# Optimization experiments

Hardware: AMD Instinct MI355X
Metric: run time of the kernel (lower is better)

Reference implementation:

```python
import math
import jax, jax.numpy as jnp
import numpy as np

N_HEAD = 16
N_HEAD_KV = 4
HEAD_DIM = 64
WINDOW = 512  # (window, 0) sliding-window causal, as in flash_attn window_size
ROPE_BASE = 10000.0


def _rope(x):
    """Rotate-half RoPE. x: (B, T, H, D)."""
    T, D = x.shape[1], x.shape[3]
    half = D // 2
    inv_freq = 1.0 / (ROPE_BASE ** (jnp.arange(half, dtype=jnp.float32) / half))
    ang = jnp.arange(T, dtype=jnp.float32)[:, None] * inv_freq[None, :]  # (T, half)
    cos = jnp.concatenate([jnp.cos(ang), jnp.cos(ang)], axis=-1)[None, :, None, :]
    sin = jnp.concatenate([jnp.sin(ang), jnp.sin(ang)], axis=-1)[None, :, None, :]
    x1, x2 = jnp.split(x, 2, axis=-1)
    rot = jnp.concatenate([-x2, x1], axis=-1)
    return x * cos.astype(x.dtype) + rot * sin.astype(x.dtype)


def setup_inputs() -> dict:
    key = jax.random.key(0)
    ks = jax.random.split(key, 7)
    B, T, C = 2, 2048, 1024
    Ckv = N_HEAD_KV * HEAD_DIM
    x = jax.random.normal(ks[0], (B, T, C), dtype=jnp.float32)
    seq_lengths = jax.random.randint(ks[1], (B,), T // 2, T + 1, dtype=jnp.int32)
    s = 0.02
    Wq = jax.random.normal(ks[2], (C, C), dtype=jnp.float32) * s
    Wk = jax.random.normal(ks[3], (C, Ckv), dtype=jnp.float32) * s
    Wv = jax.random.normal(ks[4], (C, Ckv), dtype=jnp.float32) * s
    Wo = jax.random.normal(ks[5], (C, C), dtype=jnp.float32) * s
    return {"x": x, "seq_lengths": seq_lengths, "Wq": Wq, "Wk": Wk, "Wv": Wv, "Wo": Wo}


def reference(x, seq_lengths, Wq, Wk, Wv, Wo):
    B, T, C = x.shape
    scale = 1.0 / math.sqrt(HEAD_DIM)
    q = (x @ Wq).reshape(B, T, N_HEAD, HEAD_DIM)
    k = (x @ Wk).reshape(B, T, N_HEAD_KV, HEAD_DIM)
    v = (x @ Wv).reshape(B, T, N_HEAD_KV, HEAD_DIM)
    q = _rope(q)
    k = _rope(k)
    # GQA: repeat_interleave KV heads up to N_HEAD
    rep = N_HEAD // N_HEAD_KV
    k = jnp.repeat(k, rep, axis=2)
    v = jnp.repeat(v, rep, axis=2)
    scores = jnp.einsum("bqhd,bkhd->bhqk", q, k) * scale  # (B,H,T,T)
    pos = jnp.arange(T)
    causal = pos[None, :] <= pos[:, None]                      # k <= q
    window = pos[None, :] >= (pos[:, None] - WINDOW)           # k >= q - W
    key_valid = pos[None, :] < seq_lengths[:, None]            # (B,T)
    mask = (causal & window)[None, None, :, :] & key_valid[:, None, None, :]
    scores = jnp.where(mask, scores, jnp.float32(-1e9))
    attn = jax.nn.softmax(scores, axis=-1)
    out = jnp.einsum("bhqk,bkhd->bqhd", attn, v)
    # padded query positions are zeroed (pad_input semantics in the varlen path)
    q_valid = (pos[None, :] < seq_lengths[:, None]).astype(out.dtype)
    out = out * q_valid[:, :, None, None]
    return out.reshape(B, T, C) @ Wo
```

## Files before the change

kernel.cpp:

```cpp
#include <hip/hip_runtime.h>


using bf16x8 = __attribute__((ext_vector_type(8))) short;
using f32x4  = __attribute__((ext_vector_type(4))) float;

#define B_   2
#define T_   2048
#define H_   16
#define HKV_ 4
#define D_   64
#define WIN_ 512

#define QSCALE_ 0.18033688011112042f
#define LOG2_1E4_OVER32_ 0.41524101186092029f

__device__ __forceinline__ unsigned short f2b(float f) {
  union { float f; unsigned u; } v; v.f = f;
  unsigned r = v.u + 0x7FFFu + ((v.u >> 16) & 1u);
  return (unsigned short)(r >> 16);
}
__device__ __forceinline__ unsigned short f2b_fast(float f) {
  union { float f; unsigned u; } v; v.f = f;
  return (unsigned short)((v.u + 0x8000u) >> 16);
}

typedef const __attribute__((address_space(1))) void* gas_ptr;
typedef __attribute__((address_space(3))) void* las_ptr;
__device__ __forceinline__ void gl_lds16(const void* g, void* l) {
  __builtin_amdgcn_global_load_lds((gas_ptr)g, (las_ptr)l, 16, 0, 0);
}

__global__ __launch_bounds__(256) void prep_kernel(
    const float* __restrict__ x,
    const float* __restrict__ Wq, const float* __restrict__ Wk,
    const float* __restrict__ Wv, const float* __restrict__ Wo,
    unsigned short* __restrict__ xb,
    unsigned short* __restrict__ wqT, unsigned short* __restrict__ wkT,
    unsigned short* __restrict__ wvT, unsigned short* __restrict__ woT) {
  int bx = blockIdx.x;
  if (bx < 4096) {
    int i = bx * 256 + threadIdx.x;
    float4 v = ((const float4*)x)[i];
    ushort4 o; o.x = f2b(v.x); o.y = f2b(v.y); o.z = f2b(v.z); o.w = f2b(v.w);
    ((ushort4*)xb)[i] = o;
    return;
  }
  int id = bx - 4096;
  const float* W; unsigned short* WT; int N, n0, k0;
  if (id < 1024)      { W = Wq; WT = wqT; N = 1024; }
  else if (id < 2048) { W = Wo; WT = woT; N = 1024; id -= 1024; }
  else if (id < 2304) { W = Wk; WT = wkT; N = 256;  id -= 2048; }
  else                { W = Wv; WT = wvT; N = 256;  id -= 2304; }
  if (N == 1024) { n0 = (id & 31) * 32; k0 = (id >> 5) * 32; }
  else           { n0 = (id & 7)  * 32; k0 = (id >> 3) * 32; }
  __shared__ float tile[32][33];
  int tx = threadIdx.x & 31, ty = threadIdx.x >> 5;
#pragma unroll
  for (int yy = 0; yy < 32; yy += 8)
    tile[ty + yy][tx] = W[(size_t)(k0 + ty + yy) * N + n0 + tx];
  __syncthreads();
#pragma unroll
  for (int yy = 0; yy < 32; yy += 8)
    WT[(size_t)(n0 + ty + yy) * 1024 + k0 + tx] = f2b(tile[tx][ty + yy]);
}

__global__ __launch_bounds__(256) void gemm_qkv(
    const unsigned short* __restrict__ A,
    const unsigned short* __restrict__ WqT,
    const unsigned short* __restrict__ WkT,
    const unsigned short* __restrict__ WvT,
    unsigned short* __restrict__ qb,
    unsigned short* __restrict__ kbuf,
    unsigned short* __restrict__ vbT) {
  const int K = 1024;
  __shared__ unsigned short lA[2][64 * 64];
  __shared__ unsigned short lB[2][128 * 64];
  int tid = threadIdx.x, l = tid & 63, w = tid >> 6;
  int wr = w >> 1, wc = w & 1;
  int m0 = blockIdx.x * 64;
  int n0 = blockIdx.y * 128;
  const unsigned short* Bt; int nloc;
  if (n0 < 1024)      { Bt = WqT; nloc = n0; }
  else if (n0 < 1280) { Bt = WkT; nloc = n0 - 1024; }
  else                { Bt = WvT; nloc = n0 - 1280; }

  f32x4 acc[2][4] = {};

  int scol = (((l & 7) ^ (l >> 3)) << 3);
  const unsigned short* ga = A  + (size_t)(m0   + w * 16 + (l >> 3)) * K + scol;
  const unsigned short* gb = Bt + (size_t)(nloc + w * 32 + (l >> 3)) * K + scol;

#define STG(BUF, KOFF)                                                         \
  {                                                                            \
    gl_lds16(ga + (KOFF),                  &lA[BUF][(w * 16) * 64]);           \
    gl_lds16(ga + 8 * K + (KOFF),          &lA[BUF][(w * 16 + 8) * 64]);       \
    _Pragma("unroll")                                                          \
    for (int j = 0; j < 4; ++j)                                                \
      gl_lds16(gb + j * 8 * K + (KOFF),    &lB[BUF][(w * 32 + j * 8) * 64]);   \
  }

  STG(0, 0)
  for (int it = 0; it < 16; ++it) {
    int buf = it & 1;
    if (it < 15) {
      STG(buf ^ 1, (it + 1) * 64)
      asm volatile("s_waitcnt vmcnt(6)" ::: "memory");
    } else {
      asm volatile("s_waitcnt vmcnt(0)" ::: "memory");
    }
    __builtin_amdgcn_sched_barrier(0);
    __builtin_amdgcn_s_barrier();

    bf16x8 af[2][2], bfr[4][2];
#pragma unroll
    for (int mf = 0; mf < 2; ++mf) {
      int row = wr * 32 + mf * 16 + (l & 15);
#pragma unroll
      for (int ks = 0; ks < 2; ++ks)
        af[mf][ks] = *(const bf16x8*)(
            &lA[buf][row * 64 + (((ks * 4 + (l >> 4)) ^ (row & 7)) << 3)]);
    }
#pragma unroll
    for (int nf = 0; nf < 4; ++nf) {
      int row = wc * 64 + nf * 16 + (l & 15);
#pragma unroll
      for (int ks = 0; ks < 2; ++ks)
        bfr[nf][ks] = *(const bf16x8*)(
            &lB[buf][row * 64 + (((ks * 4 + (l >> 4)) ^ (row & 7)) << 3)]);
    }
    __builtin_amdgcn_s_setprio(1);
#pragma unroll
    for (int mf = 0; mf < 2; ++mf)
#pragma unroll
      for (int nf = 0; nf < 4; ++nf) {
        acc[mf][nf] = __builtin_amdgcn_mfma_f32_16x16x32_bf16(af[mf][0], bfr[nf][0], acc[mf][nf], 0, 0, 0);
        acc[mf][nf] = __builtin_amdgcn_mfma_f32_16x16x32_bf16(af[mf][1], bfr[nf][1], acc[mf][nf], 0, 0, 0);
      }
    __builtin_amdgcn_s_setprio(0);
    __builtin_amdgcn_s_barrier();
  }
#undef STG

  int colbase = n0 + wc * 64;
  int rowbase = m0 + wr * 32;

  if (n0 < 1280) {
    float qs = (n0 < 1024) ? QSCALE_ : 1.0f;
#pragma unroll
    for (int nf = 0; nf < 2; ++nf) {
      int dd = nf * 16 + (l & 15);
      float inv = exp2f(-(float)dd * LOG2_1E4_OVER32_);
#pragma unroll
      for (int mf = 0; mf < 2; ++mf) {
#pragma unroll
        for (int i = 0; i < 4; ++i) {
          int t = (rowbase + mf * 16 + ((l >> 4) << 2) + i) & 2047;
          float sn, cs;
          __sincosf((float)t * inv, &sn, &cs);
          float x1 = acc[mf][nf][i], x2 = acc[mf][nf + 2][i];
          acc[mf][nf][i]     = (x1 * cs - x2 * sn) * qs;
          acc[mf][nf + 2][i] = (x2 * cs + x1 * sn) * qs;
        }
      }
    }
  }

#pragma unroll
  for (int mf = 0; mf < 2; ++mf)
#pragma unroll
    for (int nf = 0; nf < 4; ++nf) {
      int n    = colbase + nf * 16 + (l & 15);
      int mrow = rowbase + mf * 16 + ((l >> 4) << 2);
      int b = mrow >> 11, t = mrow & 2047;
      if (n < 1024) {
        int h = n >> 6, d = n & 63;
        size_t base = ((size_t)(b * 16 + h) * 2048 + t) * 64 + d;
#pragma unroll
        for (int i = 0; i < 4; ++i) qb[base + (size_t)i * 64] = f2b(acc[mf][nf][i]);
      } else if (n < 1280) {
        int hh = (n - 1024) >> 6, d = n & 63;
        size_t base = ((size_t)(b * 4 + hh) * 2048 + t) * 64 + d;
#pragma unroll
        for (int i = 0; i < 4; ++i) kbuf[base + (size_t)i * 64] = f2b(acc[mf][nf][i]);
      } else {
        int hh = (n - 1280) >> 6, d = n & 63;
        size_t base = ((size_t)((b * 4 + hh) * 64 + d)) * 2048 + t;
        ushort4 pk;
        pk.x = f2b(acc[mf][nf][0]); pk.y = f2b(acc[mf][nf][1]);
        pk.z = f2b(acc[mf][nf][2]); pk.w = f2b(acc[mf][nf][3]);
        *(ushort4*)(&vbT[base]) = pk;
      }
    }
}

__global__ __launch_bounds__(512, 4) void attn_kernel(
    const unsigned short* __restrict__ qb,
    const unsigned short* __restrict__ kb,
    const unsigned short* __restrict__ vbT,
    const int* __restrict__ seqlen,
    unsigned short* __restrict__ att) {
  __shared__ unsigned short kl[2][64 * 64];
  __shared__ unsigned short vt[2][64 * 64];
  __shared__ unsigned short pl[8][16 * 68];

  int bx = blockIdx.x;
  int g  = bx & 7;
  int wi = bx >> 3;
  int b  = g >> 2;
  int hk = g & 3;
  int h  = hk * 4 + (wi & 3);
  int qt = wi >> 2;
  int tid = threadIdx.x, l = tid & 63, w = tid >> 6;
  int q0 = qt << 7;
  int r0 = q0 + w * 16;
  int slen = seqlen[b];

  const unsigned short* qbase = qb  + ((size_t)(b * 16 + h)  * 2048) * 64;
  const unsigned short* kbase = kb  + ((size_t)(b * 4  + hk) * 2048) * 64;
  const unsigned short* vbase = vbT + ((size_t)(b * 4  + hk) * 64)   * 2048;

  bf16x8 aq[2];
#pragma unroll
  for (int s = 0; s < 2; ++s)
    aq[s] = *(const bf16x8*)(qbase + (size_t)(r0 + (l & 15)) * 64 + s * 32 + (l >> 4) * 8);

  f32x4 o[4] = {};
  float lp[4] = {0.f, 0.f, 0.f, 0.f};

  int lo = q0 >= WIN_ ? q0 - WIN_ : 0;
  int nt = (q0 + 128 - lo) >> 6;

  int srow = (w << 3) + (l >> 3);
  int scol = (((l & 7) ^ (l >> 3)) << 3);
  const unsigned short* ksrc = kbase + (size_t)srow * 64   + scol;
  const unsigned short* vsrc = vbase + (size_t)srow * 2048 + scol;

#define STAGE(BUF, KB0)                                                        \
  {                                                                            \
    gl_lds16(ksrc + (size_t)(KB0) * 64, &kl[BUF][w * 512]);                    \
    gl_lds16(vsrc + (KB0),              &vt[BUF][w * 512]);                    \
  }

  STAGE(0, lo)
  __syncthreads();

  for (int it = 0; it < nt; ++it) {
    int kb0 = lo + (it << 6);
    int cur = it & 1;
    if (it + 1 < nt) STAGE(cur ^ 1, kb0 + 64)

    if (kb0 <= r0 + 15 && kb0 + 63 >= r0 - WIN_) {
      f32x4 sa[4];
      __builtin_amdgcn_s_setprio(1);
#pragma unroll
      for (int nf = 0; nf < 4; ++nf) {
        int row = nf * 16 + (l & 15);
        const unsigned short* kp0 =
            &kl[cur][row * 64 + (((l >> 4)       ^ (l & 7)) << 3)];
        const unsigned short* kp1 =
            &kl[cur][row * 64 + (((4 + (l >> 4)) ^ (l & 7)) << 3)];
        f32x4 z = {};
        z = __builtin_amdgcn_mfma_f32_16x16x32_bf16(aq[0], *(const bf16x8*)kp0, z, 0, 0, 0);
        z = __builtin_amdgcn_mfma_f32_16x16x32_bf16(aq[1], *(const bf16x8*)kp1, z, 0, 0, 0);
        sa[nf] = z;
      }
      __builtin_amdgcn_s_setprio(0);

      bool noMask = (kb0 + 63 <= r0) && (kb0 >= r0 - 497);
      if (!noMask) {
#pragma unroll
        for (int nf = 0; nf < 4; ++nf) {
          int key = kb0 + nf * 16 + (l & 15);
#pragma unroll
          for (int i = 0; i < 4; ++i) {
            int qr = r0 + (l >> 4) * 4 + i;
            sa[nf][i] = (key <= qr && key >= qr - WIN_) ? sa[nf][i] : -1e30f;
          }
        }
      }

#pragma unroll
      for (int nf = 0; nf < 4; ++nf)
#pragma unroll
        for (int i = 0; i < 4; ++i) {
          float p = exp2f(sa[nf][i]);
          lp[i] += p;
          pl[w][((l >> 4) * 4 + i) * 68 + nf * 16 + (l & 15)] = f2b_fast(p);
        }

      bf16x8 ap0 = *(const bf16x8*)(&pl[w][(l & 15) * 68 + (l >> 4) * 8]);
      bf16x8 ap1 = *(const bf16x8*)(&pl[w][(l & 15) * 68 + 32 + (l >> 4) * 8]);

      __builtin_amdgcn_s_setprio(1);
#pragma unroll
      for (int df = 0; df < 4; ++df) {
        int row = df * 16 + (l & 15);
        const unsigned short* vp0 =
            &vt[cur][row * 64 + (((l >> 4)       ^ (l & 7)) << 3)];
        const unsigned short* vp1 =
            &vt[cur][row * 64 + (((4 + (l >> 4)) ^ (l & 7)) << 3)];
        o[df] = __builtin_amdgcn_mfma_f32_16x16x32_bf16(ap0, *(const bf16x8*)vp0, o[df], 0, 0, 0);
        o[df] = __builtin_amdgcn_mfma_f32_16x16x32_bf16(ap1, *(const bf16x8*)vp1, o[df], 0, 0, 0);
      }
      __builtin_amdgcn_s_setprio(0);
    }
    __syncthreads();
  }
#undef STAGE

#pragma unroll
  for (int off = 1; off <= 8; off <<= 1)
#pragma unroll
    for (int i = 0; i < 4; ++i)
      lp[i] += __shfl_xor(lp[i], off);

#pragma unroll
  for (int i = 0; i < 4; ++i) {
    int r = r0 + (l >> 4) * 4 + i;
    float inv = (r < slen && lp[i] > 0.f) ? 1.0f / lp[i] : 0.f;
#pragma unroll
    for (int df = 0; df < 4; ++df)
      att[((size_t)(b * 2048 + r)) * 1024 + h * 64 + df * 16 + (l & 15)] =
          f2b(o[df][i] * inv);
  }
}

__global__ __launch_bounds__(256) void gemm_out(
    const unsigned short* __restrict__ A,
    const unsigned short* __restrict__ Bt,
    float* __restrict__ C) {
  const int K = 1024;
  __shared__ unsigned short lA[2][64 * 64];
  __shared__ unsigned short lB[2][128 * 64];
  int tid = threadIdx.x, l = tid & 63, w = tid >> 6;
  int wr = w >> 1, wc = w & 1;
  int m0 = blockIdx.x * 64;
  int n0 = blockIdx.y * 128;

  f32x4 acc[2][4] = {};

  int scol = (((l & 7) ^ (l >> 3)) << 3);
  const unsigned short* ga = A  + (size_t)(m0 + w * 16 + (l >> 3)) * K + scol;
  const unsigned short* gb = Bt + (size_t)(n0 + w * 32 + (l >> 3)) * K + scol;

#define STG(BUF, KOFF)                                                         \
  {                                                                            \
    gl_lds16(ga + (KOFF),                  &lA[BUF][(w * 16) * 64]);           \
    gl_lds16(ga + 8 * K + (KOFF),          &lA[BUF][(w * 16 + 8) * 64]);       \
    _Pragma("unroll")                                                          \
    for (int j = 0; j < 4; ++j)                                                \
      gl_lds16(gb + j * 8 * K + (KOFF),    &lB[BUF][(w * 32 + j * 8) * 64]);   \
  }

  STG(0, 0)
  for (int it = 0; it < 16; ++it) {
    int buf = it & 1;
    if (it < 15) {
      STG(buf ^ 1, (it + 1) * 64)
      asm volatile("s_waitcnt vmcnt(6)" ::: "memory");
    } else {
      asm volatile("s_waitcnt vmcnt(0)" ::: "memory");
    }
    __builtin_amdgcn_sched_barrier(0);
    __builtin_amdgcn_s_barrier();

    bf16x8 af[2][2], bfr[4][2];
#pragma unroll
    for (int mf = 0; mf < 2; ++mf) {
      int row = wr * 32 + mf * 16 + (l & 15);
#pragma unroll
      for (int ks = 0; ks < 2; ++ks)
        af[mf][ks] = *(const bf16x8*)(
            &lA[buf][row * 64 + (((ks * 4 + (l >> 4)) ^ (row & 7)) << 3)]);
    }
#pragma unroll
    for (int nf = 0; nf < 4; ++nf) {
      int row = wc * 64 + nf * 16 + (l & 15);
#pragma unroll
      for (int ks = 0; ks < 2; ++ks)
        bfr[nf][ks] = *(const bf16x8*)(
            &lB[buf][row * 64 + (((ks * 4 + (l >> 4)) ^ (row & 7)) << 3)]);
    }
    __builtin_amdgcn_s_setprio(1);
#pragma unroll
    for (int mf = 0; mf < 2; ++mf)
#pragma unroll
      for (int nf = 0; nf < 4; ++nf) {
        acc[mf][nf] = __builtin_amdgcn_mfma_f32_16x16x32_bf16(af[mf][0], bfr[nf][0], acc[mf][nf], 0, 0, 0);
        acc[mf][nf] = __builtin_amdgcn_mfma_f32_16x16x32_bf16(af[mf][1], bfr[nf][1], acc[mf][nf], 0, 0, 0);
      }
    __builtin_amdgcn_s_setprio(0);
    __builtin_amdgcn_s_barrier();
  }
#undef STG

  int colbase = n0 + wc * 64;
  int rowbase = m0 + wr * 32;
#pragma unroll
  for (int mf = 0; mf < 2; ++mf)
#pragma unroll
    for (int nf = 0; nf < 4; ++nf) {
      int n    = colbase + nf * 16 + (l & 15);
      int mrow = rowbase + mf * 16 + ((l >> 4) << 2);
#pragma unroll
      for (int i = 0; i < 4; ++i)
        C[(size_t)(mrow + i) * 1024 + n] = acc[mf][nf][i];
    }
}

extern "C" void kernel_launch(void* const* d_in, const int* in_sizes, int n_in,
                              void* d_out, int out_size, void* d_ws, size_t ws_size,
                              hipStream_t stream) {
  const float* x  = (const float*)d_in[0];
  const int*   sl = (const int*)d_in[1];
  const float* Wq = (const float*)d_in[2];
  const float* Wk = (const float*)d_in[3];
  const float* Wv = (const float*)d_in[4];
  const float* Wo = (const float*)d_in[5];
  float* out = (float*)d_out;

  char* p = (char*)d_ws;
  unsigned short* xb  = (unsigned short*)p; p += (size_t)4096 * 1024 * 2;
  unsigned short* wqT = (unsigned short*)p; p += (size_t)1024 * 1024 * 2;
  unsigned short* wkT = (unsigned short*)p; p += (size_t)256  * 1024 * 2;
  unsigned short* wvT = (unsigned short*)p; p += (size_t)256  * 1024 * 2;
  unsigned short* woT = (unsigned short*)p; p += (size_t)1024 * 1024 * 2;
  unsigned short* qb  = (unsigned short*)p; p += (size_t)B_ * H_   * T_ * D_ * 2;
  unsigned short* kbf = (unsigned short*)p; p += (size_t)B_ * HKV_ * T_ * D_ * 2;
  unsigned short* vbT = (unsigned short*)p; p += (size_t)B_ * HKV_ * D_ * T_ * 2;
  unsigned short* att = (unsigned short*)p; p += (size_t)4096 * 1024 * 2;

  prep_kernel<<<6656, 256, 0, stream>>>(x, Wq, Wk, Wv, Wo, xb, wqT, wkT, wvT, woT);
  gemm_qkv<<<dim3(64, 12), 256, 0, stream>>>(xb, wqT, wkT, wvT, qb, kbf, vbT);
  attn_kernel<<<512, 512, 0, stream>>>(qb, kbf, vbT, sl, att);
  gemm_out<<<dim3(64, 8), 256, 0, stream>>>(att, woT, out);
}
```

Measured before the change: 69.47 us.

## Skip padded rows in projection GEMMs and attention using sequence lengths

Each GEMM block whose 64-row tile starts at or beyond its batch's sequence length skips the K loop and its RoPE epilogue, storing zero accumulators instead. The attention kernel zero-fills its output and returns early for query tiles entirely past the sequence length, and caps the key-tile loop at the last valid row. The attention loop also swaps __syncthreads for explicit vmcnt waits plus s_barrier, so the next K/V tile's load stays in flight while the current one is used. The aim is to avoid computing rows that the reference masks or zeroes. The cost is extra branching and a dependence on seqlen inside every kernel.

```diff
diff --git a/kernel.cpp b/kernel.cpp
--- a/kernel.cpp
+++ b/kernel.cpp
@@ -69,6 +69,7 @@
     const unsigned short* __restrict__ WqT,
     const unsigned short* __restrict__ WkT,
     const unsigned short* __restrict__ WvT,
+    const int* __restrict__ seqlen,
     unsigned short* __restrict__ qb,
     unsigned short* __restrict__ kbuf,
     unsigned short* __restrict__ vbT) {
@@ -85,6 +86,7 @@
   else                { Bt = WvT; nloc = n0 - 1280; }
 
   f32x4 acc[2][4] = {};
+  bool dead = (m0 & 2047) >= seqlen[m0 >> 11];
 
   int scol = (((l & 7) ^ (l >> 3)) << 3);
   const unsigned short* ga = A  + (size_t)(m0   + w * 16 + (l >> 3)) * K + scol;
@@ -99,52 +101,54 @@
       gl_lds16(gb + j * 8 * K + (KOFF),    &lB[BUF][(w * 32 + j * 8) * 64]);   \
   }
 
-  STG(0, 0)
-  for (int it = 0; it < 16; ++it) {
-    int buf = it & 1;
-    if (it < 15) {
-      STG(buf ^ 1, (it + 1) * 64)
-      asm volatile("s_waitcnt vmcnt(6)" ::: "memory");
-    } else {
-      asm volatile("s_waitcnt vmcnt(0)" ::: "memory");
-    }
-    __builtin_amdgcn_sched_barrier(0);
-    __builtin_amdgcn_s_barrier();
-
-    bf16x8 af[2][2], bfr[4][2];
-#pragma unroll
-    for (int mf = 0; mf < 2; ++mf) {
-      int row = wr * 32 + mf * 16 + (l & 15);
-#pragma unroll
-      for (int ks = 0; ks < 2; ++ks)
-        af[mf][ks] = *(const bf16x8*)(
-            &lA[buf][row * 64 + (((ks * 4 + (l >> 4)) ^ (row & 7)) << 3)]);
-    }
-#pragma unroll
-    for (int nf = 0; nf < 4; ++nf) {
-      int row = wc * 64 + nf * 16 + (l & 15);
-#pragma unroll
-      for (int ks = 0; ks < 2; ++ks)
-        bfr[nf][ks] = *(const bf16x8*)(
-            &lB[buf][row * 64 + (((ks * 4 + (l >> 4)) ^ (row & 7)) << 3)]);
-    }
-    __builtin_amdgcn_s_setprio(1);
-#pragma unroll
-    for (int mf = 0; mf < 2; ++mf)
+  if (!dead) {
+    STG(0, 0)
+    for (int it = 0; it < 16; ++it) {
+      int buf = it & 1;
+      if (it < 15) {
+        STG(buf ^ 1, (it + 1) * 64)
+        asm volatile("s_waitcnt vmcnt(6)" ::: "memory");
+      } else {
+        asm volatile("s_waitcnt vmcnt(0)" ::: "memory");
+      }
+      __builtin_amdgcn_sched_barrier(0);
+      __builtin_amdgcn_s_barrier();
+
+      bf16x8 af[2][2], bfr[4][2];
+#pragma unroll
+      for (int mf = 0; mf < 2; ++mf) {
+        int row = wr * 32 + mf * 16 + (l & 15);
+#pragma unroll
+        for (int ks = 0; ks < 2; ++ks)
+          af[mf][ks] = *(const bf16x8*)(
+              &lA[buf][row * 64 + (((ks * 4 + (l >> 4)) ^ (row & 7)) << 3)]);
+      }
 #pragma unroll
       for (int nf = 0; nf < 4; ++nf) {
-        acc[mf][nf] = __builtin_amdgcn_mfma_f32_16x16x32_bf16(af[mf][0], bfr[nf][0], acc[mf][nf], 0, 0, 0);
-        acc[mf][nf] = __builtin_amdgcn_mfma_f32_16x16x32_bf16(af[mf][1], bfr[nf][1], acc[mf][nf], 0, 0, 0);
-      }
-    __builtin_amdgcn_s_setprio(0);
-    __builtin_amdgcn_s_barrier();
+        int row = wc * 64 + nf * 16 + (l & 15);
+#pragma unroll
+        for (int ks = 0; ks < 2; ++ks)
+          bfr[nf][ks] = *(const bf16x8*)(
+              &lB[buf][row * 64 + (((ks * 4 + (l >> 4)) ^ (row & 7)) << 3)]);
+      }
+      __builtin_amdgcn_s_setprio(1);
+#pragma unroll
+      for (int mf = 0; mf < 2; ++mf)
+#pragma unroll
+        for (int nf = 0; nf < 4; ++nf) {
+          acc[mf][nf] = __builtin_amdgcn_mfma_f32_16x16x32_bf16(af[mf][0], bfr[nf][0], acc[mf][nf], 0, 0, 0);
+          acc[mf][nf] = __builtin_amdgcn_mfma_f32_16x16x32_bf16(af[mf][1], bfr[nf][1], acc[mf][nf], 0, 0, 0);
+        }
+      __builtin_amdgcn_s_setprio(0);
+      __builtin_amdgcn_s_barrier();
+    }
   }
 #undef STG
 
   int colbase = n0 + wc * 64;
   int rowbase = m0 + wr * 32;
 
-  if (n0 < 1280) {
+  if (n0 < 1280 && !dead) {
     float qs = (n0 < 1024) ? QSCALE_ : 1.0f;
 #pragma unroll
     for (int nf = 0; nf < 2; ++nf) {
@@ -215,6 +219,16 @@
   int r0 = q0 + w * 16;
   int slen = seqlen[b];
 
+  if (q0 >= slen) {
+    int r = q0 + (tid >> 2);
+    int c = (tid & 3) * 16;
+    size_t base = ((size_t)(b * 2048 + r)) * 1024 + h * 64 + c;
+    ushort4 z = {0, 0, 0, 0};
+#pragma unroll
+    for (int j = 0; j < 4; ++j) *(ushort4*)(&att[base + j * 4]) = z;
+    return;
+  }
+
   const unsigned short* qbase = qb  + ((size_t)(b * 16 + h)  * 2048) * 64;
   const unsigned short* kbase = kb  + ((size_t)(b * 4  + hk) * 2048) * 64;
   const unsigned short* vbase = vbT + ((size_t)(b * 4  + hk) * 64)   * 2048;
@@ -228,7 +242,8 @@
   float lp[4] = {0.f, 0.f, 0.f, 0.f};
 
   int lo = q0 >= WIN_ ? q0 - WIN_ : 0;
-  int nt = (q0 + 128 - lo) >> 6;
+  int hi_row = min(q0 + 127, slen - 1);
+  int nt = ((hi_row - lo) >> 6) + 1;
 
   int srow = (w << 3) + (l >> 3);
   int scol = (((l & 7) ^ (l >> 3)) << 3);
@@ -242,12 +257,18 @@
   }
 
   STAGE(0, lo)
-  __syncthreads();
 
   for (int it = 0; it < nt; ++it) {
     int kb0 = lo + (it << 6);
     int cur = it & 1;
-    if (it + 1 < nt) STAGE(cur ^ 1, kb0 + 64)
+    if (it + 1 < nt) {
+      STAGE(cur ^ 1, kb0 + 64)
+      asm volatile("s_waitcnt vmcnt(2)" ::: "memory");
+    } else {
+      asm volatile("s_waitcnt vmcnt(0)" ::: "memory");
+    }
+    __builtin_amdgcn_sched_barrier(0);
+    __builtin_amdgcn_s_barrier();
 
     if (kb0 <= r0 + 15 && kb0 + 63 >= r0 - WIN_) {
       f32x4 sa[4];
@@ -304,7 +325,7 @@
       }
       __builtin_amdgcn_s_setprio(0);
     }
-    __syncthreads();
+    __builtin_amdgcn_s_barrier();
   }
 #undef STAGE
 
@@ -328,6 +349,7 @@
 __global__ __launch_bounds__(256) void gemm_out(
     const unsigned short* __restrict__ A,
     const unsigned short* __restrict__ Bt,
+    const int* __restrict__ seqlen,
     float* __restrict__ C) {
   const int K = 1024;
   __shared__ unsigned short lA[2][64 * 64];
@@ -338,6 +360,7 @@
   int n0 = blockIdx.y * 128;
 
   f32x4 acc[2][4] = {};
+  bool dead = (m0 & 2047) >= seqlen[m0 >> 11];
 
   int scol = (((l & 7) ^ (l >> 3)) << 3);
   const unsigned short* ga = A  + (size_t)(m0 + w * 16 + (l >> 3)) * K + scol;
@@ -352,45 +375,47 @@
       gl_lds16(gb + j * 8 * K + (KOFF),    &lB[BUF][(w * 32 + j * 8) * 64]);   \
   }
 
-  STG(0, 0)
-  for (int it = 0; it < 16; ++it) {
-    int buf = it & 1;
-    if (it < 15) {
-      STG(buf ^ 1, (it + 1) * 64)
-      asm volatile("s_waitcnt vmcnt(6)" ::: "memory");
-    } else {
-      asm volatile("s_waitcnt vmcnt(0)" ::: "memory");
-    }
-    __builtin_amdgcn_sched_barrier(0);
-    __builtin_amdgcn_s_barrier();
-
-    bf16x8 af[2][2], bfr[4][2];
-#pragma unroll
-    for (int mf = 0; mf < 2; ++mf) {
-      int row = wr * 32 + mf * 16 + (l & 15);
-#pragma unroll
-      for (int ks = 0; ks < 2; ++ks)
-        af[mf][ks] = *(const bf16x8*)(
-            &lA[buf][row * 64 + (((ks * 4 + (l >> 4)) ^ (row & 7)) << 3)]);
-    }
-#pragma unroll
-    for (int nf = 0; nf < 4; ++nf) {
-      int row = wc * 64 + nf * 16 + (l & 15);
-#pragma unroll
-      for (int ks = 0; ks < 2; ++ks)
-        bfr[nf][ks] = *(const bf16x8*)(
-            &lB[buf][row * 64 + (((ks * 4 + (l >> 4)) ^ (row & 7)) << 3)]);
-    }
-    __builtin_amdgcn_s_setprio(1);
-#pragma unroll
-    for (int mf = 0; mf < 2; ++mf)
+  if (!dead) {
+    STG(0, 0)
+    for (int it = 0; it < 16; ++it) {
+      int buf = it & 1;
+      if (it < 15) {
+        STG(buf ^ 1, (it + 1) * 64)
+        asm volatile("s_waitcnt vmcnt(6)" ::: "memory");
+      } else {
+        asm volatile("s_waitcnt vmcnt(0)" ::: "memory");
+      }
+      __builtin_amdgcn_sched_barrier(0);
+      __builtin_amdgcn_s_barrier();
+
+      bf16x8 af[2][2], bfr[4][2];
+#pragma unroll
+      for (int mf = 0; mf < 2; ++mf) {
+        int row = wr * 32 + mf * 16 + (l & 15);
+#pragma unroll
+        for (int ks = 0; ks < 2; ++ks)
+          af[mf][ks] = *(const bf16x8*)(
+              &lA[buf][row * 64 + (((ks * 4 + (l >> 4)) ^ (row & 7)) << 3)]);
+      }
 #pragma unroll
       for (int nf = 0; nf < 4; ++nf) {
-        acc[mf][nf] = __builtin_amdgcn_mfma_f32_16x16x32_bf16(af[mf][0], bfr[nf][0], acc[mf][nf], 0, 0, 0);
-        acc[mf][nf] = __builtin_amdgcn_mfma_f32_16x16x32_bf16(af[mf][1], bfr[nf][1], acc[mf][nf], 0, 0, 0);
-      }
-    __builtin_amdgcn_s_setprio(0);
-    __builtin_amdgcn_s_barrier();
+        int row = wc * 64 + nf * 16 + (l & 15);
+#pragma unroll
+        for (int ks = 0; ks < 2; ++ks)
+          bfr[nf][ks] = *(const bf16x8*)(
+              &lB[buf][row * 64 + (((ks * 4 + (l >> 4)) ^ (row & 7)) << 3)]);
+      }
+      __builtin_amdgcn_s_setprio(1);
+#pragma unroll
+      for (int mf = 0; mf < 2; ++mf)
+#pragma unroll
+        for (int nf = 0; nf < 4; ++nf) {
+          acc[mf][nf] = __builtin_amdgcn_mfma_f32_16x16x32_bf16(af[mf][0], bfr[nf][0], acc[mf][nf], 0, 0, 0);
+          acc[mf][nf] = __builtin_amdgcn_mfma_f32_16x16x32_bf16(af[mf][1], bfr[nf][1], acc[mf][nf], 0, 0, 0);
+        }
+      __builtin_amdgcn_s_setprio(0);
+      __builtin_amdgcn_s_barrier();
+    }
   }
 #undef STG
 
@@ -431,7 +456,7 @@
   unsigned short* att = (unsigned short*)p; p += (size_t)4096 * 1024 * 2;
 
   prep_kernel<<<6656, 256, 0, stream>>>(x, Wq, Wk, Wv, Wo, xb, wqT, wkT, wvT, woT);
-  gemm_qkv<<<dim3(64, 12), 256, 0, stream>>>(xb, wqT, wkT, wvT, qb, kbf, vbT);
+  gemm_qkv<<<dim3(64, 12), 256, 0, stream>>>(xb, wqT, wkT, wvT, sl, qb, kbf, vbT);
   attn_kernel<<<512, 512, 0, stream>>>(qb, kbf, vbT, sl, att);
-  gemm_out<<<dim3(64, 8), 256, 0, stream>>>(att, woT, out);
-}
+  gemm_out<<<dim3(64, 8), 256, 0, stream>>>(att, woT, sl, out);
+}
```

New measurement: 69.80 us. Within noise of the previous version (+0.5%).
